# Kernel tuning notes

Hardware: AMD Instinct MI355X
Metric: run time of the kernel (lower is better)

## Reference

```python
import jax, jax.numpy as jnp
import numpy as np

B, C, H, W = 8, 128, 64, 64
D_STATE = 16
D_CONV = 4
EXPAND = 1.25
D_INNER = int(EXPAND * C)        # 160
DT_RANK = int(np.ceil(C / 16))   # 8


def setup_inputs() -> dict:
    key = jax.random.key(0)
    ks = jax.random.split(key, 10)
    f = lambda k, s, sc=0.02: jax.random.normal(k, s, dtype=jnp.float32) * sc
    return {
        "x": jax.random.normal(ks[0], (B, C, H, W), dtype=jnp.float32),
        "ln_g": jnp.ones((C,), jnp.float32),
        "ln_b": jnp.zeros((C,), jnp.float32),
        "in_proj_w": f(ks[1], (2 * D_INNER, C)),
        "conv_w": f(ks[2], (D_INNER, 1, D_CONV)),            # depthwise causal conv kernel
        "conv_b": jnp.zeros((D_INNER,), jnp.float32),
        "x_proj_w": f(ks[3], (DT_RANK + 2 * D_STATE, D_INNER)),
        "dt_proj_w": f(ks[4], (D_INNER, DT_RANK), 0.1),
        "dt_proj_b": f(ks[5], (D_INNER,), 0.1),
        # S4-style init: A_log = log(1..d_state) per inner channel (frozen in torch module)
        "A_log": jnp.log(jnp.tile(jnp.arange(1, D_STATE + 1, dtype=jnp.float32), (D_INNER, 1))),
        "D_param": jnp.ones((D_INNER,), jnp.float32),
        "out_proj_w": f(ks[6], (C, D_INNER)),
        "fuse_w": f(ks[7], (C, 2 * C)),                      # 1x1 conv == per-token matmul
        "scale": jnp.ones((1,), jnp.float32) * 0.1,
    }


def _layernorm(x, g, b, eps=1e-5):
    m = x.mean(-1, keepdims=True)
    v = x.var(-1, keepdims=True)
    return (x - m) * jax.lax.rsqrt(v + eps) * g + b


def _mamba(seq, in_proj_w, conv_w, conv_b, x_proj_w, dt_proj_w, dt_proj_b,
           A_log, D_param, out_proj_w):
    # seq: (B, L, C)
    Bsz, L, _ = seq.shape
    xz = jnp.einsum('blc,ec->ble', seq, in_proj_w)           # (B, L, 2*d_inner)
    xm, z = jnp.split(xz, 2, axis=-1)
    # depthwise causal conv over L, truncated to L (padding = d_conv-1 on the left)
    xc = jax.lax.conv_general_dilated(
        xm.transpose(0, 2, 1), conv_w, (1,), [(D_CONV - 1, 0)],
        feature_group_count=D_INNER, dimension_numbers=('NCH', 'OIH', 'NCH'))
    xm = jax.nn.silu((xc + conv_b[None, :, None]).transpose(0, 2, 1))  # (B, L, d_inner)
    x_dbl = jnp.einsum('bld,ed->ble', xm, x_proj_w)
    dt = x_dbl[..., :DT_RANK]
    Bm = x_dbl[..., DT_RANK:DT_RANK + D_STATE]               # (B, L, d_state)
    Cm = x_dbl[..., DT_RANK + D_STATE:]                      # (B, L, d_state)
    dt = jax.nn.softplus(jnp.einsum('blr,dr->bld', dt, dt_proj_w) + dt_proj_b)
    A = -jnp.exp(A_log)                                      # (d_inner, d_state)

    def step(h, inp):
        dt_t, B_t, C_t, x_t = inp                            # (B,d) (B,n) (B,n) (B,d)
        dA = jnp.exp(dt_t[:, :, None] * A)                   # (B, d_inner, d_state)
        h = dA * h + (dt_t * x_t)[:, :, None] * B_t[:, None, :]
        y = jnp.einsum('bdn,bn->bd', h, C_t)
        return h, y

    h0 = jnp.zeros((Bsz, D_INNER, D_STATE), dtype=seq.dtype)
    xs = (dt.transpose(1, 0, 2), Bm.transpose(1, 0, 2),
          Cm.transpose(1, 0, 2), xm.transpose(1, 0, 2))
    _, ys = jax.lax.scan(step, h0, xs)                       # ys: (L, B, d_inner)
    y = ys.transpose(1, 0, 2) + xm * D_param
    y = y * jax.nn.silu(z)
    return jnp.einsum('bld,cd->blc', y, out_proj_w)          # (B, L, C)


def reference(x, ln_g, ln_b, in_proj_w, conv_w, conv_b, x_proj_w, dt_proj_w,
              dt_proj_b, A_log, D_param, out_proj_w, fuse_w, scale):
    Bsz, Ch, Hh, Ww = x.shape
    seq = x.reshape(Bsz, Ch, Hh * Ww).transpose(0, 2, 1)     # (B, L, C) raster order
    seq_n = _layernorm(seq, ln_g, ln_b)                      # LN is per-token: commutes with flip
    args = (in_proj_w, conv_w, conv_b, x_proj_w, dt_proj_w, dt_proj_b,
            A_log, D_param, out_proj_w)
    y0 = _mamba(seq_n, *args)                                # forward raster scan
    y1 = _mamba(seq_n[:, ::-1, :], *args)[:, ::-1, :]        # reversed raster scan
    fused = jnp.einsum('blk,ck->blc', jnp.concatenate([y0, y1], axis=-1), fuse_w)
    out = seq + scale * fused                                # residual + learned scale
    return out.transpose(0, 2, 1).reshape(Bsz, Ch, Hh, Ww)
```

## Files before the change

### kernel.cpp

```cpp
#include <hip/hip_runtime.h>
#include <math.h>

#define LSEQ   4096
#define BATCH  8
#define CDIM   128
#define DIN    160
#define DSTATE 16
#define DTRANK 8
#define BLROWS (BATCH*LSEQ)
#define NCHUNK 128
#define TCH    32
#define SUBC   8
#define NSEG   16

typedef __attribute__((ext_vector_type(8))) short short8;
typedef __attribute__((ext_vector_type(8))) __bf16 bf16x8;
typedef __attribute__((ext_vector_type(4))) float float4v;

__device__ __forceinline__ float4v mfma_bf16(short8 a, short8 b, float4v c) {
  return __builtin_amdgcn_mfma_f32_16x16x32_bf16(
      __builtin_bit_cast(bf16x8, a), __builtin_bit_cast(bf16x8, b), c, 0, 0, 0);
}

__device__ __forceinline__ unsigned short f2bf(float f) {
  union { float f; unsigned u; } v; v.f = f;
  unsigned r = v.u + 0x7FFF + ((v.u >> 16) & 1);
  return (unsigned short)(r >> 16);
}
__device__ __forceinline__ float bf2f(unsigned short h) {
  union { unsigned u; float f; } v; v.u = ((unsigned)h) << 16;
  return v.f;
}

__global__ void prep_weights(const float* __restrict__ inpw, const float* __restrict__ xpw,
                             const float* __restrict__ fuse_w, const float* __restrict__ out_proj_w,
                             unsigned short* __restrict__ inpw_bf, unsigned short* __restrict__ xpw_bf,
                             unsigned short* __restrict__ W01) {
  int i = blockIdx.x * 256 + threadIdx.x;
  if (i < 320 * 128) inpw_bf[i] = f2bf(inpw[i]);
  if (i < 40 * 160)  xpw_bf[i]  = f2bf(xpw[i]);
  if (i < CDIM * DIN) {
    int d = i % DIN, c = i / DIN;
    float a0 = 0.f, a1 = 0.f;
    for (int k = 0; k < CDIM; ++k) {
      float o = out_proj_w[k * DIN + d];
      a0 += fuse_w[c * 256 + k] * o;
      a1 += fuse_w[c * 256 + 128 + k] * o;
    }
    W01[c * DIN + d] = f2bf(a0);
    W01[CDIM * DIN + c * DIN + d] = f2bf(a1);
  }
}

__global__ void ln_transpose_kernel(const float* __restrict__ x,
                                    const float* __restrict__ g,
                                    const float* __restrict__ bb,
                                    unsigned short* __restrict__ seqn) {
  __shared__ float sA[128 * 65];
  __shared__ float psum[2 * 256];
  __shared__ float mrs[2 * 64];
  int l0 = blockIdx.x * 64;
  int b  = blockIdx.y;
  int t  = threadIdx.x;
  int lsub = t & 63, crow = t >> 6;
  const float* xb = x + (size_t)b * CDIM * LSEQ;
  for (int it = 0; it < 32; ++it) {
    int c = crow + it * 4;
    sA[c * 65 + lsub] = xb[(size_t)c * LSEQ + l0 + lsub];
  }
  __syncthreads();
  float s = 0.f, ss = 0.f;
  for (int j = 0; j < 32; ++j) {
    int c = crow * 32 + j;
    float v = sA[c * 65 + lsub];
    s += v; ss += v * v;
  }
  psum[crow * 64 + lsub] = s;
  psum[256 + crow * 64 + lsub] = ss;
  __syncthreads();
  if (t < 64) {
    float su = 0.f, sq = 0.f;
    for (int p = 0; p < 4; ++p) { su += psum[p * 64 + t]; sq += psum[256 + p * 64 + t]; }
    float m = su * (1.f / 128.f);
    float var = sq * (1.f / 128.f) - m * m;
    mrs[t] = m;
    mrs[64 + t] = rsqrtf(var + 1e-5f);
  }
  __syncthreads();
  int c = t & 127, half = t >> 7;
  float gc = g[c], bc = bb[c];
  for (int it = 0; it < 32; ++it) {
    int l = it * 2 + half;
    float v = (sA[c * 65 + l] - mrs[l]) * mrs[64 + l] * gc + bc;
    seqn[((size_t)(b * LSEQ + l0 + l)) * CDIM + c] = f2bf(v);
  }
}

template<int K, bool MASKN, bool BF16OUT>
__global__ __launch_bounds__(256)
void gemm_mfma(const unsigned short* __restrict__ A0, const unsigned short* __restrict__ A1,
               const unsigned short* __restrict__ W,
               void* __restrict__ C0, void* __restrict__ C1, int N) {
  constexpr int LSTR = K + 8;
  __shared__ __align__(16) unsigned short As[64 * LSTR];
  __shared__ __align__(16) unsigned short Ws[64 * LSTR];
  const unsigned short* A = blockIdx.z ? A1 : A0;
  void* Cp = blockIdx.z ? C1 : C0;
  int m0 = blockIdx.x * 64;
  int n0 = blockIdx.y * 64;
  int t = threadIdx.x;
  constexpr int CH = 64 * K / 8;
  for (int c = t; c < CH; c += 256) {
    int row = c / (K / 8);
    int col = (c % (K / 8)) * 8;
    *(short8*)&As[row * LSTR + col] = *(const short8*)&A[(size_t)(m0 + row) * K + col];
    short8 wv = {};
    int nr = n0 + row;
    if (!MASKN || nr < N) wv = *(const short8*)&W[(size_t)nr * K + col];
    *(short8*)&Ws[row * LSTR + col] = wv;
  }
  __syncthreads();
  int lane = t & 63;
  int w = t >> 6;
  int l15 = lane & 15, quad = lane >> 4;
  float4v acc[4] = {};
#pragma unroll
  for (int kk = 0; kk < K; kk += 32) {
    short8 bfrag = *(const short8*)&Ws[(w * 16 + l15) * LSTR + kk + quad * 8];
#pragma unroll
    for (int i = 0; i < 4; ++i) {
      short8 afrag = *(const short8*)&As[(i * 16 + l15) * LSTR + kk + quad * 8];
      acc[i] = mfma_bf16(afrag, bfrag, acc[i]);
    }
  }
  int col = n0 + w * 16 + l15;
  if (MASKN && col >= N) return;
#pragma unroll
  for (int i = 0; i < 4; ++i)
#pragma unroll
    for (int r = 0; r < 4; ++r) {
      int row = m0 + i * 16 + quad * 4 + r;
      if (BF16OUT) ((unsigned short*)Cp)[(size_t)row * N + col] = f2bf(acc[i][r]);
      else         ((float*)Cp)[(size_t)row * N + col] = acc[i][r];
    }
}

__global__ void conv_silu_kernel(const unsigned short* __restrict__ xz,
                                 const float* __restrict__ cw,
                                 const float* __restrict__ cb,
                                 unsigned short* __restrict__ xm0,
                                 unsigned short* __restrict__ xm1) {
  int idx = blockIdx.x * 256 + threadIdx.x;
  int dir = blockIdx.y;
  if (idx >= BLROWS * 80) return;
  int dp = idx % 80;
  int bl = idx / 80;
  int l = bl % LSEQ, b = bl / LSEQ;
  int d = dp * 2;
  float w0[4], w1[4];
#pragma unroll
  for (int k = 0; k < 4; ++k) { w0[k] = cw[d * 4 + k]; w1[k] = cw[d * 4 + 4 + k]; }
  float a0 = cb[d], a1 = cb[d + 1];
  const unsigned short* base = xz + ((size_t)b * LSEQ) * 320 + d;
  if (dir == 0) {
#pragma unroll
    for (int k = 0; k < 4; ++k) {
      int lp = l - 3 + k;
      if (lp >= 0) {
        unsigned v = *(const unsigned*)&base[(size_t)lp * 320];
        a0 += w0[k] * bf2f((unsigned short)v);
        a1 += w1[k] * bf2f((unsigned short)(v >> 16));
      }
    }
  } else {
#pragma unroll
    for (int k = 0; k < 4; ++k) {
      int lp = l + 3 - k;
      if (lp < LSEQ) {
        unsigned v = *(const unsigned*)&base[(size_t)lp * 320];
        a0 += w0[k] * bf2f((unsigned short)v);
        a1 += w1[k] * bf2f((unsigned short)(v >> 16));
      }
    }
  }
  float s0 = a0 / (1.f + __expf(-a0));
  float s1 = a1 / (1.f + __expf(-a1));
  unsigned outv = (unsigned)f2bf(s0) | ((unsigned)f2bf(s1) << 16);
  unsigned short* xm = dir ? xm1 : xm0;
  *(unsigned*)&xm[(size_t)bl * DIN + d] = outv;
}

__device__ __forceinline__ void decay_powers(float r1, float* dA) {
  float r2 = r1 * r1;
  float r4 = r2 * r2;
  float r8 = r4 * r4;
  dA[0] = r1;       dA[1] = r2;       dA[2] = r2 * r1;  dA[3] = r4;
  dA[4] = r4 * r1;  dA[5] = r4 * r2;  dA[6] = r4 * dA[2]; dA[7] = r8;
  dA[8] = r8 * r1;  dA[9] = r8 * r2;  dA[10] = r8 * dA[2]; dA[11] = r8 * r4;
  dA[12] = r8 * dA[4]; dA[13] = r8 * dA[5]; dA[14] = r8 * dA[6]; dA[15] = r8 * r8;
}

__device__ __forceinline__ const float* uniform_row(const float* base, int elem_off) {
  return base + __builtin_amdgcn_readfirstlane(elem_off);
}

__global__ void scan_passA(const float* __restrict__ xdbl0, const float* __restrict__ xdbl1,
                           const unsigned short* __restrict__ xm0v, const unsigned short* __restrict__ xm1v,
                           const float* __restrict__ dt_w, const float* __restrict__ dt_b,
                           const float* __restrict__ Dp,
                           float* __restrict__ Q, float* __restrict__ dtsum,
                           _Float16* __restrict__ rc0, _Float16* __restrict__ rc1,
                           unsigned short* __restrict__ y0, unsigned short* __restrict__ y1) {
  int chunk = blockIdx.x, b = blockIdx.y, dir = blockIdx.z;
  int t = threadIdx.x;
  if (t >= DIN) return;
  const float* xdbl = dir ? xdbl1 : xdbl0;
  const unsigned short* xm = dir ? xm1v : xm0v;
  _Float16* rc = dir ? rc1 : rc0;
  unsigned short* yl = dir ? y1 : y0;
  int d = t;
  float dw[8];
#pragma unroll
  for (int r = 0; r < 8; ++r) dw[r] = dt_w[d * 8 + r];
  float db = dt_b[d];
  float Dd = Dp[d];
  float h[16];
#pragma unroll
  for (int n = 0; n < 16; ++n) h[n] = 0.f;
  float cum = 0.f;
  float rcum = 1.f;
#pragma unroll 4
  for (int tt = 0; tt < TCH; ++tt) {
    int pos = chunk * TCH + tt;
    int l = dir ? (LSEQ - 1 - pos) : pos;
    int rowi = b * LSEQ + l;
    const float* xr = uniform_row(xdbl, rowi * 40);
    float xmv = bf2f(xm[(size_t)rowi * DIN + d]);
    float zz = db;
#pragma unroll
    for (int r = 0; r < 8; ++r) zz += xr[r] * dw[r];
    float e  = __expf(fminf(zz, 20.f));
    float dt = (zz > 20.f) ? zz : __logf(1.f + e);
    float r1 = 1.f / (1.f + e);
    cum += dt;
    rcum *= r1;
    rc[(size_t)rowi * DIN + d] = (_Float16)rcum;
    float u = dt * xmv;
    float dA[16];
    decay_powers(r1, dA);
    float y = xmv * Dd;
#pragma unroll
    for (int n = 0; n < 16; ++n) {
      h[n] = dA[n] * h[n] + u * xr[8 + n];
      y += h[n] * xr[24 + n];
    }
    yl[(size_t)rowi * DIN + d] = f2bf(y);
  }
  size_t base = (size_t)((dir * BATCH + b) * NCHUNK + chunk);
#pragma unroll
  for (int n = 0; n < 16; ++n) Q[base * (DIN * 16) + d * 16 + n] = h[n];
  dtsum[base * DIN + d] = cum;
}

__global__ __launch_bounds__(256)
void scan_passB(const float* __restrict__ Q, const float* __restrict__ dtsum,
                float* __restrict__ Hinit) {
  __shared__ float sA[NSEG * 16], sQ[NSEG * 16];
  int blk = blockIdx.x;
  int d = blk % DIN;
  int rem = blk / DIN;
  int t = threadIdx.x;
  int n = t & 15, cs = t >> 4;
  float An = -(float)(n + 1);
  float a[SUBC], q[SUBC];
  float Aseg = 1.f, Qseg = 0.f;
#pragma unroll
  for (int j = 0; j < SUBC; ++j) {
    int ch = cs * SUBC + j;
    size_t base = (size_t)rem * NCHUNK + ch;
    float dsv = dtsum[base * DIN + d];
    float av = __expf(An * dsv);
    float qv = Q[base * (DIN * 16) + d * 16 + n];
    a[j] = av; q[j] = qv;
    Qseg = av * Qseg + qv;
    Aseg *= av;
  }
  sA[cs * 16 + n] = Aseg;
  sQ[cs * 16 + n] = Qseg;
  __syncthreads();
  if (t < 16) {
    float h = 0.f;
    for (int s = 0; s < NSEG; ++s) {
      float Av = sA[s * 16 + t], Qv = sQ[s * 16 + t];
      sA[s * 16 + t] = h;
      h = Av * h + Qv;
    }
  }
  __syncthreads();
  float h = sA[cs * 16 + n];
#pragma unroll
  for (int j = 0; j < SUBC; ++j) {
    int ch = cs * SUBC + j;
    size_t base = (size_t)rem * NCHUNK + ch;
    Hinit[base * (DIN * 16) + d * 16 + n] = h;
    h = a[j] * h + q[j];
  }
}

__global__ void scan_passC(const float* __restrict__ xdbl0, const float* __restrict__ xdbl1,
                           const unsigned short* __restrict__ xz,
                           const float* __restrict__ Hinit,
                           const _Float16* __restrict__ rc0, const _Float16* __restrict__ rc1,
                           const unsigned short* __restrict__ yl0, const unsigned short* __restrict__ yl1,
                           unsigned short* __restrict__ yg0, unsigned short* __restrict__ yg1) {
  int chunk = blockIdx.x, b = blockIdx.y, dir = blockIdx.z;
  int t = threadIdx.x;
  if (t >= DIN) return;
  const float* xdbl = dir ? xdbl1 : xdbl0;
  const _Float16* rc = dir ? rc1 : rc0;
  const unsigned short* yl = dir ? yl1 : yl0;
  unsigned short* yg = dir ? yg1 : yg0;
  int d = t;
  size_t base = (size_t)((dir * BATCH + b) * NCHUNK + chunk);
  float H0[16];
#pragma unroll
  for (int n = 0; n < 16; ++n) H0[n] = Hinit[base * (DIN * 16) + d * 16 + n];
#pragma unroll 2
  for (int tt = 0; tt < TCH; ++tt) {
    int pos = chunk * TCH + tt;
    int l = dir ? (LSEQ - 1 - pos) : pos;
    int rowi = b * LSEQ + l;
    const float* xr = uniform_row(xdbl, rowi * 40 + 24);
    size_t di = (size_t)rowi * DIN + d;
    float y = bf2f(yl[di]);
    float rcum = (float)rc[di];
    float zv = bf2f(xz[(size_t)rowi * 320 + 160 + d]);
    float dA[16];
    decay_powers(rcum, dA);
    float corr = 0.f;
#pragma unroll
    for (int n = 0; n < 16; ++n) corr += xr[n] * dA[n] * H0[n];
    y += corr;
    float sz = zv / (1.f + __expf(-zv));
    yg[di] = f2bf(y * sz);
  }
}

__global__ __launch_bounds__(256)
void final_mfma(const unsigned short* __restrict__ yg0, const unsigned short* __restrict__ yg1,
                const unsigned short* __restrict__ W01, const float* __restrict__ x,
                const float* __restrict__ scale, float* __restrict__ out) {
  constexpr int K = DIN, LSTR = K + 8;
  __shared__ __align__(16) unsigned short As[64 * LSTR];
  __shared__ __align__(16) unsigned short Ws[64 * LSTR];
  float* sC = (float*)As;
  int m0 = blockIdx.x * 64;
  int c0 = blockIdx.y * 64;
  int b = m0 / LSEQ, l0 = m0 % LSEQ;
  int t = threadIdx.x;
  int lane = t & 63;
  int w = t >> 6;
  int l15 = lane & 15, quad = lane >> 4;
  float4v acc[4] = {};
  for (int pass = 0; pass < 2; ++pass) {
    const unsigned short* A = pass ? yg1 : yg0;
    const unsigned short* W = W01 + pass * (CDIM * K);
    if (pass) __syncthreads();
    constexpr int CH = 64 * K / 8;
    for (int c = t; c < CH; c += 256) {
      int row = c / (K / 8);
      int col = (c % (K / 8)) * 8;
      *(short8*)&As[row * LSTR + col] = *(const short8*)&A[(size_t)(m0 + row) * K + col];
      *(short8*)&Ws[row * LSTR + col] = *(const short8*)&W[(size_t)(c0 + row) * K + col];
    }
    __syncthreads();
#pragma unroll
    for (int kk = 0; kk < K; kk += 32) {
      short8 bfrag = *(const short8*)&Ws[(w * 16 + l15) * LSTR + kk + quad * 8];
#pragma unroll
      for (int i = 0; i < 4; ++i) {
        short8 afrag = *(const short8*)&As[(i * 16 + l15) * LSTR + kk + quad * 8];
        acc[i] = mfma_bf16(afrag, bfrag, acc[i]);
      }
    }
  }
  __syncthreads();
#pragma unroll
  for (int i = 0; i < 4; ++i)
#pragma unroll
    for (int r = 0; r < 4; ++r)
      sC[(i * 16 + quad * 4 + r) * 65 + w * 16 + l15] = acc[i][r];
  __syncthreads();
  float sc = scale[0];
  int ll = t & 63, cq = t >> 6;
#pragma unroll
  for (int j = 0; j < 16; ++j) {
    int cl = cq * 16 + j;
    float v = sC[ll * 65 + cl];
    size_t gi = ((size_t)(b * CDIM + c0 + cl)) * LSEQ + l0 + ll;
    out[gi] = x[gi] + sc * v;
  }
}

extern "C" void kernel_launch(void* const* d_in, const int* in_sizes, int n_in,
                              void* d_out, int out_size, void* d_ws, size_t ws_size,
                              hipStream_t stream) {
  const float* x        = (const float*)d_in[0];
  const float* ln_g     = (const float*)d_in[1];
  const float* ln_b     = (const float*)d_in[2];
  const float* in_projw = (const float*)d_in[3];
  const float* conv_w   = (const float*)d_in[4];
  const float* conv_b   = (const float*)d_in[5];
  const float* x_projw  = (const float*)d_in[6];
  const float* dt_projw = (const float*)d_in[7];
  const float* dt_projb = (const float*)d_in[8];
  const float* A_log    = (const float*)d_in[9];
  const float* D_param  = (const float*)d_in[10];
  const float* out_projw= (const float*)d_in[11];
  const float* fuse_w   = (const float*)d_in[12];
  const float* scale    = (const float*)d_in[13];
  float* out = (float*)d_out;
  (void)A_log;

  float* ws = (float*)d_ws;
  size_t off = 0;
  unsigned short* seqn_bf = (unsigned short*)(ws + off); off += (size_t)BLROWS * CDIM / 2;
  unsigned short* xz      = (unsigned short*)(ws + off); off += (size_t)BLROWS * 320 / 2;
  unsigned short* xm0 = (unsigned short*)(ws + off); off += (size_t)BLROWS * DIN / 2;
  unsigned short* xm1 = (unsigned short*)(ws + off); off += (size_t)BLROWS * DIN / 2;
  float* xdbl0 = ws + off; off += (size_t)BLROWS * 40;
  float* xdbl1 = ws + off; off += (size_t)BLROWS * 40;
  float* Q     = ws + off; off += (size_t)2 * BATCH * NCHUNK * DIN * 16;
  float* Hinit = ws + off; off += (size_t)2 * BATCH * NCHUNK * DIN * 16;
  float* dtsum = ws + off; off += (size_t)2 * BATCH * NCHUNK * DIN;
  _Float16* rc0 = (_Float16*)(ws + off); off += (size_t)BLROWS * DIN / 2;
  _Float16* rc1 = (_Float16*)(ws + off); off += (size_t)BLROWS * DIN / 2;
  unsigned short* yl0 = (unsigned short*)(ws + off); off += (size_t)BLROWS * DIN / 2;
  unsigned short* yl1 = (unsigned short*)(ws + off); off += (size_t)BLROWS * DIN / 2;
  unsigned short* yg0 = (unsigned short*)(ws + off); off += (size_t)BLROWS * DIN / 2;
  unsigned short* yg1 = (unsigned short*)(ws + off); off += (size_t)BLROWS * DIN / 2;
  unsigned short* W01bf = (unsigned short*)(ws + off); off += (size_t)2 * CDIM * DIN / 2;
  unsigned short* inpw_bf = (unsigned short*)(ws + off); off += (size_t)320 * 128 / 2;
  unsigned short* xpw_bf  = (unsigned short*)(ws + off); off += (size_t)40 * 160 / 2 + 8;

  prep_weights<<<(320 * 128 + 255) / 256, 256, 0, stream>>>(
      in_projw, x_projw, fuse_w, out_projw, inpw_bf, xpw_bf, W01bf);
  ln_transpose_kernel<<<dim3(LSEQ / 64, BATCH), 256, 0, stream>>>(x, ln_g, ln_b, seqn_bf);
  gemm_mfma<128, false, true><<<dim3(BLROWS / 64, 5, 1), 256, 0, stream>>>(
      seqn_bf, seqn_bf, inpw_bf, xz, xz, 320);
  conv_silu_kernel<<<dim3((BLROWS * 80 + 255) / 256, 2), 256, 0, stream>>>(xz, conv_w, conv_b, xm0, xm1);
  gemm_mfma<160, true, false><<<dim3(BLROWS / 64, 1, 2), 256, 0, stream>>>(
      xm0, xm1, xpw_bf, xdbl0, xdbl1, 40);
  scan_passA<<<dim3(NCHUNK, BATCH, 2), 192, 0, stream>>>(xdbl0, xdbl1, xm0, xm1,
                                                         dt_projw, dt_projb, D_param,
                                                         Q, dtsum, rc0, rc1, yl0, yl1);
  scan_passB<<<2 * BATCH * DIN, 256, 0, stream>>>(Q, dtsum, Hinit);
  scan_passC<<<dim3(NCHUNK, BATCH, 2), 192, 0, stream>>>(xdbl0, xdbl1, xz, Hinit,
                                                         rc0, rc1, yl0, yl1, yg0, yg1);
  final_mfma<<<dim3(BLROWS / 64, CDIM / 64), 256, 0, stream>>>(yg0, yg1, W01bf, x, scale, out);
}
```

Before: 251.1 us.

## Halve scan chunk length, stage rows in LDS, pack y/rcum, precompute silu(z)

Chunk length is halved and the chunk count doubled, so the first and third scan passes launch twice as many blocks. Both passes now cooperatively stage their per-chunk xdbl, xm, y/rcum and gate rows into shared memory before the sequential loop, replacing per-timestep global loads. The local y and rcum are packed into one 32-bit word. silu(z) is computed once in the conv kernel and stored as fp16, and Hinit aliases Q in place. In exchange this adds an extra global buffer, an fp16 store of the gate, and doubles the carry traffic in the middle pass.

New measurement: 267.0 us. +6.4%, slower.

```diff
diff --git a/kernel.cpp b/kernel.cpp
--- a/kernel.cpp
+++ b/kernel.cpp
@@ -8,9 +8,9 @@
 #define DSTATE 16
 #define DTRANK 8
 #define BLROWS (BATCH*LSEQ)
-#define NCHUNK 128
-#define TCH    32
-#define SUBC   8
+#define NCHUNK 256
+#define TCH    16
+#define SUBC   16
 #define NSEG   16
 
 typedef __attribute__((ext_vector_type(8))) short short8;
@@ -149,7 +149,8 @@
                                  const float* __restrict__ cw,
                                  const float* __restrict__ cb,
                                  unsigned short* __restrict__ xm0,
-                                 unsigned short* __restrict__ xm1) {
+                                 unsigned short* __restrict__ xm1,
+                                 _Float16* __restrict__ szp) {
   int idx = blockIdx.x * 256 + threadIdx.x;
   int dir = blockIdx.y;
   if (idx >= BLROWS * 80) return;
@@ -188,6 +189,15 @@
   unsigned outv = (unsigned)f2bf(s0) | ((unsigned)f2bf(s1) << 16);
   unsigned short* xm = dir ? xm1 : xm0;
   *(unsigned*)&xm[(size_t)bl * DIN + d] = outv;
+  if (dir == 0) {
+    unsigned zv = *(const unsigned*)&xz[(size_t)bl * 320 + 160 + d];
+    float z0 = bf2f((unsigned short)zv), z1 = bf2f((unsigned short)(zv >> 16));
+    float g0 = z0 / (1.f + __expf(-z0));
+    float g1 = z1 / (1.f + __expf(-z1));
+    unsigned short h0 = __builtin_bit_cast(unsigned short, (_Float16)g0);
+    unsigned short h1 = __builtin_bit_cast(unsigned short, (_Float16)g1);
+    *(unsigned*)&szp[(size_t)bl * DIN + d] = (unsigned)h0 | ((unsigned)h1 << 16);
+  }
 }
 
 __device__ __forceinline__ void decay_powers(float r1, float* dA) {
@@ -200,24 +210,33 @@
   dA[12] = r8 * dA[4]; dA[13] = r8 * dA[5]; dA[14] = r8 * dA[6]; dA[15] = r8 * r8;
 }
 
-__device__ __forceinline__ const float* uniform_row(const float* base, int elem_off) {
-  return base + __builtin_amdgcn_readfirstlane(elem_off);
-}
-
-__global__ void scan_passA(const float* __restrict__ xdbl0, const float* __restrict__ xdbl1,
-                           const unsigned short* __restrict__ xm0v, const unsigned short* __restrict__ xm1v,
-                           const float* __restrict__ dt_w, const float* __restrict__ dt_b,
-                           const float* __restrict__ Dp,
-                           float* __restrict__ Q, float* __restrict__ dtsum,
-                           _Float16* __restrict__ rc0, _Float16* __restrict__ rc1,
-                           unsigned short* __restrict__ y0, unsigned short* __restrict__ y1) {
+__global__ __launch_bounds__(192, 6)
+void scan_passA(const float* __restrict__ xdbl0, const float* __restrict__ xdbl1,
+                const unsigned short* __restrict__ xm0v, const unsigned short* __restrict__ xm1v,
+                const float* __restrict__ dt_w, const float* __restrict__ dt_b,
+                const float* __restrict__ Dp,
+                float* __restrict__ Q, float* __restrict__ dtsum,
+                unsigned* __restrict__ yr0, unsigned* __restrict__ yr1) {
+  __shared__ __align__(16) float sx[TCH * 40];
+  __shared__ __align__(16) unsigned short sxm[TCH * DIN];
   int chunk = blockIdx.x, b = blockIdx.y, dir = blockIdx.z;
   int t = threadIdx.x;
-  if (t >= DIN) return;
   const float* xdbl = dir ? xdbl1 : xdbl0;
   const unsigned short* xm = dir ? xm1v : xm0v;
-  _Float16* rc = dir ? rc1 : rc0;
-  unsigned short* yl = dir ? y1 : y0;
+  unsigned* yr = dir ? yr1 : yr0;
+  int l00 = dir ? (LSEQ - 1 - chunk * TCH) : (chunk * TCH);
+  int step = dir ? -1 : 1;
+  int rowbase = b * LSEQ + l00;
+  for (int i = t; i < TCH * 40; i += 192) {
+    int tt = i / 40, j = i - tt * 40;
+    sx[i] = xdbl[(size_t)(rowbase + step * tt) * 40 + j];
+  }
+  for (int i = t; i < TCH * (DIN / 2); i += 192) {
+    int tt = i / 80, j = i - tt * 80;
+    ((unsigned*)sxm)[i] = *(const unsigned*)&xm[(size_t)(rowbase + step * tt) * DIN + 2 * j];
+  }
+  __syncthreads();
+  if (t >= DIN) return;
   int d = t;
   float dw[8];
 #pragma unroll
@@ -229,32 +248,31 @@
   for (int n = 0; n < 16; ++n) h[n] = 0.f;
   float cum = 0.f;
   float rcum = 1.f;
+  unsigned* yrp = yr + (size_t)rowbase * DIN + d;
 #pragma unroll 4
   for (int tt = 0; tt < TCH; ++tt) {
-    int pos = chunk * TCH + tt;
-    int l = dir ? (LSEQ - 1 - pos) : pos;
-    int rowi = b * LSEQ + l;
-    const float* xr = uniform_row(xdbl, rowi * 40);
-    float xmv = bf2f(xm[(size_t)rowi * DIN + d]);
+    const float* xrow = &sx[tt * 40];
+    float xmv = bf2f(sxm[tt * DIN + d]);
     float zz = db;
 #pragma unroll
-    for (int r = 0; r < 8; ++r) zz += xr[r] * dw[r];
+    for (int r = 0; r < 8; ++r) zz += xrow[r] * dw[r];
     float e  = __expf(fminf(zz, 20.f));
     float dt = (zz > 20.f) ? zz : __logf(1.f + e);
     float r1 = 1.f / (1.f + e);
     cum += dt;
     rcum *= r1;
-    rc[(size_t)rowi * DIN + d] = (_Float16)rcum;
     float u = dt * xmv;
     float dA[16];
     decay_powers(r1, dA);
     float y = xmv * Dd;
 #pragma unroll
     for (int n = 0; n < 16; ++n) {
-      h[n] = dA[n] * h[n] + u * xr[8 + n];
-      y += h[n] * xr[24 + n];
-    }
-    yl[(size_t)rowi * DIN + d] = f2bf(y);
+      h[n] = dA[n] * h[n] + u * xrow[8 + n];
+      y += h[n] * xrow[24 + n];
+    }
+    unsigned short rch = __builtin_bit_cast(unsigned short, (_Float16)rcum);
+    *yrp = (unsigned)f2bf(y) | ((unsigned)rch << 16);
+    yrp += step * DIN;
   }
   size_t base = (size_t)((dir * BATCH + b) * NCHUNK + chunk);
 #pragma unroll
@@ -263,8 +281,8 @@
 }
 
 __global__ __launch_bounds__(256)
-void scan_passB(const float* __restrict__ Q, const float* __restrict__ dtsum,
-                float* __restrict__ Hinit) {
+void scan_passB(const float* Q, const float* __restrict__ dtsum,
+                float* Hinit) {
   __shared__ float sA[NSEG * 16], sQ[NSEG * 16];
   int blk = blockIdx.x;
   int d = blk % DIN;
@@ -307,42 +325,57 @@
   }
 }
 
-__global__ void scan_passC(const float* __restrict__ xdbl0, const float* __restrict__ xdbl1,
-                           const unsigned short* __restrict__ xz,
-                           const float* __restrict__ Hinit,
-                           const _Float16* __restrict__ rc0, const _Float16* __restrict__ rc1,
-                           const unsigned short* __restrict__ yl0, const unsigned short* __restrict__ yl1,
-                           unsigned short* __restrict__ yg0, unsigned short* __restrict__ yg1) {
+__global__ __launch_bounds__(192, 6)
+void scan_passC(const float* __restrict__ xdbl0, const float* __restrict__ xdbl1,
+                const _Float16* __restrict__ szp,
+                const float* __restrict__ Hinit,
+                const unsigned* __restrict__ yr0, const unsigned* __restrict__ yr1,
+                unsigned short* __restrict__ yg0, unsigned short* __restrict__ yg1) {
+  __shared__ __align__(16) float sC[TCH * 16];
+  __shared__ __align__(16) unsigned syr[TCH * DIN];
+  __shared__ __align__(16) _Float16 ssz[TCH * DIN];
   int chunk = blockIdx.x, b = blockIdx.y, dir = blockIdx.z;
   int t = threadIdx.x;
+  const float* xdbl = dir ? xdbl1 : xdbl0;
+  const unsigned* yrb = dir ? yr1 : yr0;
+  unsigned short* yg = dir ? yg1 : yg0;
+  int l00 = dir ? (LSEQ - 1 - chunk * TCH) : (chunk * TCH);
+  int step = dir ? -1 : 1;
+  int rowbase = b * LSEQ + l00;
+  for (int i = t; i < TCH * 16; i += 192) {
+    int tt = i >> 4, j = i & 15;
+    sC[i] = xdbl[(size_t)(rowbase + step * tt) * 40 + 24 + j];
+  }
+  for (int i = t; i < TCH * DIN; i += 192) {
+    int tt = i / DIN, j = i - tt * DIN;
+    syr[i] = yrb[(size_t)(rowbase + step * tt) * DIN + j];
+  }
+  for (int i = t; i < TCH * (DIN / 2); i += 192) {
+    int tt = i / 80, j = i - tt * 80;
+    ((unsigned*)ssz)[i] = *(const unsigned*)&szp[(size_t)(rowbase + step * tt) * DIN + 2 * j];
+  }
+  __syncthreads();
   if (t >= DIN) return;
-  const float* xdbl = dir ? xdbl1 : xdbl0;
-  const _Float16* rc = dir ? rc1 : rc0;
-  const unsigned short* yl = dir ? yl1 : yl0;
-  unsigned short* yg = dir ? yg1 : yg0;
   int d = t;
   size_t base = (size_t)((dir * BATCH + b) * NCHUNK + chunk);
   float H0[16];
 #pragma unroll
   for (int n = 0; n < 16; ++n) H0[n] = Hinit[base * (DIN * 16) + d * 16 + n];
-#pragma unroll 2
+  unsigned short* ygp = yg + (size_t)rowbase * DIN + d;
+#pragma unroll 4
   for (int tt = 0; tt < TCH; ++tt) {
-    int pos = chunk * TCH + tt;
-    int l = dir ? (LSEQ - 1 - pos) : pos;
-    int rowi = b * LSEQ + l;
-    const float* xr = uniform_row(xdbl, rowi * 40 + 24);
-    size_t di = (size_t)rowi * DIN + d;
-    float y = bf2f(yl[di]);
-    float rcum = (float)rc[di];
-    float zv = bf2f(xz[(size_t)rowi * 320 + 160 + d]);
+    unsigned v = syr[tt * DIN + d];
+    float y = bf2f((unsigned short)v);
+    float rcum = (float)__builtin_bit_cast(_Float16, (unsigned short)(v >> 16));
+    float sz = (float)ssz[tt * DIN + d];
+    const float* cr = &sC[tt * 16];
     float dA[16];
     decay_powers(rcum, dA);
     float corr = 0.f;
 #pragma unroll
-    for (int n = 0; n < 16; ++n) corr += xr[n] * dA[n] * H0[n];
-    y += corr;
-    float sz = zv / (1.f + __expf(-zv));
-    yg[di] = f2bf(y * sz);
+    for (int n = 0; n < 16; ++n) corr += cr[n] * (dA[n] * H0[n]);
+    *ygp = f2bf((y + corr) * sz);
+    ygp += step * DIN;
   }
 }
 
@@ -431,14 +464,13 @@
   float* xdbl0 = ws + off; off += (size_t)BLROWS * 40;
   float* xdbl1 = ws + off; off += (size_t)BLROWS * 40;
   float* Q     = ws + off; off += (size_t)2 * BATCH * NCHUNK * DIN * 16;
-  float* Hinit = ws + off; off += (size_t)2 * BATCH * NCHUNK * DIN * 16;
+  float* Hinit = Q;
   float* dtsum = ws + off; off += (size_t)2 * BATCH * NCHUNK * DIN;
-  _Float16* rc0 = (_Float16*)(ws + off); off += (size_t)BLROWS * DIN / 2;
-  _Float16* rc1 = (_Float16*)(ws + off); off += (size_t)BLROWS * DIN / 2;
-  unsigned short* yl0 = (unsigned short*)(ws + off); off += (size_t)BLROWS * DIN / 2;
-  unsigned short* yl1 = (unsigned short*)(ws + off); off += (size_t)BLROWS * DIN / 2;
+  unsigned* yr0 = (unsigned*)(ws + off); off += (size_t)BLROWS * DIN;
+  unsigned* yr1 = (unsigned*)(ws + off); off += (size_t)BLROWS * DIN;
   unsigned short* yg0 = (unsigned short*)(ws + off); off += (size_t)BLROWS * DIN / 2;
   unsigned short* yg1 = (unsigned short*)(ws + off); off += (size_t)BLROWS * DIN / 2;
+  _Float16* szv = (_Float16*)(ws + off); off += (size_t)BLROWS * DIN / 2;
   unsigned short* W01bf = (unsigned short*)(ws + off); off += (size_t)2 * CDIM * DIN / 2;
   unsigned short* inpw_bf = (unsigned short*)(ws + off); off += (size_t)320 * 128 / 2;
   unsigned short* xpw_bf  = (unsigned short*)(ws + off); off += (size_t)40 * 160 / 2 + 8;
@@ -448,14 +480,15 @@
   ln_transpose_kernel<<<dim3(LSEQ / 64, BATCH), 256, 0, stream>>>(x, ln_g, ln_b, seqn_bf);
   gemm_mfma<128, false, true><<<dim3(BLROWS / 64, 5, 1), 256, 0, stream>>>(
       seqn_bf, seqn_bf, inpw_bf, xz, xz, 320);
-  conv_silu_kernel<<<dim3((BLROWS * 80 + 255) / 256, 2), 256, 0, stream>>>(xz, conv_w, conv_b, xm0, xm1);
+  conv_silu_kernel<<<dim3((BLROWS * 80 + 255) / 256, 2), 256, 0, stream>>>(
+      xz, conv_w, conv_b, xm0, xm1, szv);
   gemm_mfma<160, true, false><<<dim3(BLROWS / 64, 1, 2), 256, 0, stream>>>(
       xm0, xm1, xpw_bf, xdbl0, xdbl1, 40);
   scan_passA<<<dim3(NCHUNK, BATCH, 2), 192, 0, stream>>>(xdbl0, xdbl1, xm0, xm1,
                                                          dt_projw, dt_projb, D_param,
-                                                         Q, dtsum, rc0, rc1, yl0, yl1);
+                                                         Q, dtsum, yr0, yr1);
   scan_passB<<<2 * BATCH * DIN, 256, 0, stream>>>(Q, dtsum, Hinit);
-  scan_passC<<<dim3(NCHUNK, BATCH, 2), 192, 0, stream>>>(xdbl0, xdbl1, xz, Hinit,
-                                                         rc0, rc1, yl0, yl1, yg0, yg1);
+  scan_passC<<<dim3(NCHUNK, BATCH, 2), 192, 0, stream>>>(xdbl0, xdbl1, szv, Hinit,
+                                                         yr0, yr1, yg0, yg1);
   final_mfma<<<dim3(BLROWS / 64, CDIM / 64), 256, 0, stream>>>(yg0, yg1, W01bf, x, scale, out);
 }
```
